# Optimization experiments

Measured on AMD Instinct MI355X. Metric: run time of the kernel, lower is better.

Reference implementation:

```python
import jax, jax.numpy as jnp
import numpy as np
import math

B, N, FIN, FOUT, OPE = 16, 2048, 128, 128, 64


def setup_inputs() -> dict:
    key = jax.random.key(0)
    ks = jax.random.split(key, 10)
    h = jax.random.normal(ks[0], (B, N, FIN), dtype=jnp.float32)
    adj = jax.random.randint(ks[1], (B, N, N), 0, 2).astype(jnp.float32)
    op_emb = jax.random.normal(ks[2], (B, N, OPE), dtype=jnp.float32)
    # Linear weights stored as (in, out) so y = x @ W; torch init scale ~ 1/sqrt(fan_in)
    s_in = 1.0 / math.sqrt(FIN)
    Wk = jax.random.uniform(ks[3], (FIN, FOUT), minval=-s_in, maxval=s_in)
    Wq = jax.random.uniform(ks[4], (FIN, FOUT), minval=-s_in, maxval=s_in)
    Wv = jax.random.uniform(ks[5], (FIN, FOUT), minval=-s_in, maxval=s_in)
    s_a = 1.0 / math.sqrt(FOUT)
    a_w = jax.random.uniform(ks[6], (FOUT,), minval=-s_a, maxval=s_a)
    s_op = 1.0 / math.sqrt(OPE)
    op_W = jax.random.uniform(ks[7], (OPE, FOUT), minval=-s_op, maxval=s_op)
    op_b = jax.random.uniform(ks[8], (FOUT,), minval=-s_op, maxval=s_op)
    ln_g = jnp.ones((FOUT,), dtype=jnp.float32)
    ln_b = jnp.zeros((FOUT,), dtype=jnp.float32)
    return {"h": h, "adj": adj, "op_emb": op_emb, "Wk": Wk, "Wq": Wq,
            "Wv": Wv, "a_w": a_w, "op_W": op_W, "op_b": op_b,
            "ln_g": ln_g, "ln_b": ln_b}


def reference(h, adj, op_emb, Wk, Wq, Wv, a_w, op_W, op_b, ln_g, ln_b):
    d = Wk.shape[1]
    Whk = h @ Wk  # (B,N,d)
    Whq = h @ Wq
    Whv = h @ Wv
    # Original builds a_input[b,e,l,m] = Whq[b,e,m]*Whk[b,l,m] (B,N,N,d) then
    # projects with a (d->1). Algebraically: scores[b,e,l] = <Whq[b,e], Whk[b,l]*a_w>.
    scores = jnp.einsum('bed,bld->bel', Whq, Whk * a_w)
    scores = scores / jnp.sqrt(jnp.float32(d))  # attention_rescale
    alpha = jax.nn.leaky_relu(scores, negative_slope=0.2)  # leakrelu
    alpha = alpha * adj  # multiplicative mask (zeros stay in the softmax)
    attn = jax.nn.softmax(alpha, axis=-1)  # softmax over source nodes l
    agg = jnp.einsum('bel,bld->bed', attn, Whv)  # (B,N,d)
    gate = jax.nn.sigmoid(op_emb @ op_W + op_b)  # opattention branch
    hp = gate * agg
    # LayerNorm over last dim, eps=1e-5
    mu = jnp.mean(hp, axis=-1, keepdims=True)
    var = jnp.mean(jnp.square(hp - mu), axis=-1, keepdims=True)
    return (hp - mu) * jax.lax.rsqrt(var + 1e-5) * ln_g + ln_b
```

## Files before the change

kernel.cpp:

```cpp
#include <hip/hip_runtime.h>

typedef unsigned int u32;
typedef float f32x4 __attribute__((ext_vector_type(4)));
typedef short s16x8 __attribute__((ext_vector_type(8)));

#define LDA 136

#define WQT_OFF 0ULL
#define WKT_OFF 32768ULL
#define WVT_OFF 65536ULL
#define OPWT_OFF 98304ULL
#define Q_OFF 114688ULL
#define K_OFF (Q_OFF + 8388608ULL)
#define VT_OFF (K_OFF + 8388608ULL)
#define GATE_OFF (VT_OFF + 8388608ULL)

__device__ __forceinline__ u32 f2bf(float f) {
  u32 u = __float_as_uint(f);
  return (u + 0x7fffu + ((u >> 16) & 1u)) >> 16;
}

__device__ __forceinline__ void gl_lds16(const void* g, void* l) {
  __builtin_amdgcn_global_load_lds((const __attribute__((address_space(1))) void*)g,
                                   (__attribute__((address_space(3))) void*)l, 16, 0, 0);
}

__global__ void k0_wt(const float* Wq, const float* Wk, const float* Wv,
                      const float* aw, const float* opW, char* ws) {
  int nt = blockIdx.x;
  int KK = (nt == 3) ? 64 : 128;
  const float* S = (nt == 0) ? Wq : (nt == 1) ? Wk : (nt == 2) ? Wv : opW;
  unsigned short* D = (unsigned short*)(ws + (nt == 0 ? WQT_OFF : nt == 1 ? WKT_OFF : nt == 2 ? WVT_OFF : OPWT_OFF));
  for (int i = threadIdx.x; i < 128 * KK; i += blockDim.x) {
    int d = i / KK, k = i - d * KK;
    float v = S[k * 128 + d];
    if (nt == 1) v *= aw[d] * 0.12751743f;
    D[i] = (unsigned short)f2bf(v);
  }
}

__launch_bounds__(256, 2)
__global__ void k1_proj(const float* __restrict__ h, const float* __restrict__ op_emb,
                        const float* __restrict__ op_b, char* __restrict__ ws) {
  int nt = blockIdx.x, et = blockIdx.y;
  int KK = (nt == 3) ? 64 : 128;
  __shared__ unsigned short bufA[128 * LDA];
  __shared__ unsigned short bufB[128 * LDA];
  unsigned short* wbuf = (nt == 2) ? bufB : bufA;
  unsigned short* xbuf = (nt == 2) ? bufA : bufB;
  const unsigned short* Wt = (const unsigned short*)(ws + (nt == 0 ? WQT_OFF : nt == 1 ? WKT_OFF : nt == 2 ? WVT_OFF : OPWT_OFF));
  {
    const u32* Ws = (const u32*)Wt;
    int cnt = 128 * KK / 2;
    for (int i = threadIdx.x; i < cnt; i += 256) {
      int r = (2 * i) / KK, c = 2 * i - r * KK;
      *(u32*)&wbuf[r * LDA + c] = Ws[i];
    }
  }
  {
    const float* X = (nt == 3) ? (op_emb + (size_t)et * 128 * 64) : (h + (size_t)et * 128 * 128);
    int cnt = 128 * KK / 4;
    for (int i = threadIdx.x; i < cnt; i += 256) {
      float4 v = *(const float4*)(X + 4 * i);
      int r = (4 * i) / KK, c = 4 * i - r * KK;
      u32 lo = f2bf(v.x) | (f2bf(v.y) << 16);
      u32 hi = f2bf(v.z) | (f2bf(v.w) << 16);
      *(uint2*)&xbuf[r * LDA + c] = make_uint2(lo, hi);
    }
  }
  __syncthreads();
  int tid = threadIdx.x, w = tid >> 6, lane = tid & 63, l15 = lane & 15, q = lane >> 4;
  int wa = w >> 1, wb = w & 1;
  f32x4 acc[4][4];
#pragma unroll
  for (int a = 0; a < 4; a++)
#pragma unroll
    for (int bq = 0; bq < 4; bq++) acc[a][bq] = f32x4{0.f, 0.f, 0.f, 0.f};
  for (int ks = 0; ks < KK / 32; ks++) {
    s16x8 af[4], bf_[4];
#pragma unroll
    for (int mt = 0; mt < 4; mt++)
      af[mt] = *(const s16x8*)&bufA[(wa * 64 + mt * 16 + l15) * LDA + ks * 32 + q * 8];
#pragma unroll
    for (int n2 = 0; n2 < 4; n2++)
      bf_[n2] = *(const s16x8*)&bufB[(wb * 64 + n2 * 16 + l15) * LDA + ks * 32 + q * 8];
#pragma unroll
    for (int mt = 0; mt < 4; mt++)
#pragma unroll
      for (int n2 = 0; n2 < 4; n2++)
        acc[mt][n2] = __builtin_amdgcn_mfma_f32_16x16x32_bf16(af[mt], bf_[n2], acc[mt][n2], 0, 0, 0);
  }
  if (nt <= 1) {
    unsigned short* Dst = (unsigned short*)(ws + (nt == 0 ? Q_OFF : K_OFF));
#pragma unroll
    for (int mt = 0; mt < 4; mt++)
#pragma unroll
      for (int n2 = 0; n2 < 4; n2++) {
        int d0 = wa * 64 + mt * 16 + q * 4;
        int eg = et * 128 + wb * 64 + n2 * 16 + l15;
        f32x4 a = acc[mt][n2];
        u32 lo = f2bf(a[0]) | (f2bf(a[1]) << 16);
        u32 hi = f2bf(a[2]) | (f2bf(a[3]) << 16);
        *(uint2*)(Dst + (size_t)eg * 128 + d0) = make_uint2(lo, hi);
      }
  } else if (nt == 2) {
    unsigned short* Dst = (unsigned short*)(ws + VT_OFF);
    int b = et >> 4;
    int ein0 = (et & 15) * 128;
#pragma unroll
    for (int mt = 0; mt < 4; mt++)
#pragma unroll
      for (int n2 = 0; n2 < 4; n2++) {
        int e0b = ein0 + wa * 64 + mt * 16 + q * 4;
        int d = wb * 64 + n2 * 16 + l15;
        f32x4 a = acc[mt][n2];
        u32 lo = f2bf(a[0]) | (f2bf(a[1]) << 16);
        u32 hi = f2bf(a[2]) | (f2bf(a[3]) << 16);
        *(uint2*)(Dst + (size_t)b * 128 * 2048 + (size_t)d * 2048 + e0b) = make_uint2(lo, hi);
      }
  } else {
    float* Dst = (float*)(ws + GATE_OFF);
#pragma unroll
    for (int mt = 0; mt < 4; mt++)
#pragma unroll
      for (int n2 = 0; n2 < 4; n2++) {
        int d0 = wa * 64 + mt * 16 + q * 4;
        int eg = et * 128 + wb * 64 + n2 * 16 + l15;
        f32x4 a = acc[mt][n2];
        float4 g4;
        g4.x = 1.f / (1.f + __builtin_amdgcn_exp2f(-(a[0] + op_b[d0 + 0]) * 1.4426950f));
        g4.y = 1.f / (1.f + __builtin_amdgcn_exp2f(-(a[1] + op_b[d0 + 1]) * 1.4426950f));
        g4.z = 1.f / (1.f + __builtin_amdgcn_exp2f(-(a[2] + op_b[d0 + 2]) * 1.4426950f));
        g4.w = 1.f / (1.f + __builtin_amdgcn_exp2f(-(a[3] + op_b[d0 + 3]) * 1.4426950f));
        *(float4*)(Dst + (size_t)eg * 128 + d0) = g4;
      }
  }
}

__launch_bounds__(512, 2)
__global__ void k2_attn(const float* __restrict__ adj, const float* __restrict__ ln_g,
                        const float* __restrict__ ln_b, char* __restrict__ ws,
                        float* __restrict__ out) {
  __shared__ char smem[100864];
  unsigned short* Klds = (unsigned short*)smem;
  unsigned short* Vlds = (unsigned short*)(smem + 32768);
  char* PLb = smem + 65536;
  float* sden = (float*)(smem + 100352);

  const int bid = blockIdx.x;
  const int xcd = bid & 7, slot = bid >> 3;
  const int b = xcd * 2 + (slot >> 4);
  const int e0 = (slot & 15) << 7;

  const unsigned short* Qg = (const unsigned short*)(ws + Q_OFF) + ((size_t)b * 2048 + e0) * 128;
  const unsigned short* Kg = (const unsigned short*)(ws + K_OFF) + (size_t)b * 2048 * 128;
  const unsigned short* Vtg = (const unsigned short*)(ws + VT_OFF) + (size_t)b * 128 * 2048;
  const float* gateg = (const float*)(ws + GATE_OFF) + ((size_t)b * 2048 + e0) * 128;
  const float* adjg = adj + (size_t)b * 2048 * 2048 + (size_t)e0 * 2048;

  const int tid = threadIdx.x;
  const int w = tid >> 6, lane = tid & 63, l15 = lane & 15, q = lane >> 4;
  const int wh = w >> 2, we = w & 3;

  if (tid < 128) sden[tid] = 0.0f;

  s16x8 qf[2][4];
#pragma unroll
  for (int et = 0; et < 2; et++) {
    const int e = we * 32 + et * 16 + l15;
#pragma unroll
    for (int ks = 0; ks < 4; ks++)
      qf[et][ks] = *(const s16x8*)(Qg + (size_t)e * 128 + ks * 32 + q * 8);
  }

  f32x4 oacc[4][2];
#pragma unroll
  for (int dt = 0; dt < 4; dt++)
#pragma unroll
    for (int et = 0; et < 2; et++) oacc[dt][et] = f32x4{0.f, 0.f, 0.f, 0.f};
  float dp0 = 0.0f, dp1 = 0.0f;
  float4 adjA[2][4], adjB[2][4];

#pragma unroll
  for (int j = 0; j < 4; j++) {
    int S = (j * 8 + w) * 64 + lane;
    int r = S >> 4, cp = S & 15, c = cp ^ (r & 15);
    gl_lds16(Kg + (size_t)r * 128 + (c << 3), (char*)Klds + (j * 8 + w) * 1024);
    gl_lds16(Vtg + (size_t)r * 2048 + (c << 3), (char*)Vlds + (j * 8 + w) * 1024);
  }
#pragma unroll
  for (int et = 0; et < 2; et++) {
    const int e = we * 32 + et * 16 + l15;
#pragma unroll
    for (int lt = 0; lt < 4; lt++)
      adjA[et][lt] = *(const float4*)(adjg + (size_t)e * 2048 + wh * 64 + lt * 16 + q * 4);
  }

#pragma unroll 2
  for (int it = 0; it < 16; it++) {
    __syncthreads();
    if (it < 15) {
      const float* ab = adjg + (it + 1) * 128;
#pragma unroll
      for (int et = 0; et < 2; et++) {
        const int e = we * 32 + et * 16 + l15;
#pragma unroll
        for (int lt = 0; lt < 4; lt++)
          adjB[et][lt] = *(const float4*)(ab + (size_t)e * 2048 + wh * 64 + lt * 16 + q * 4);
      }
    }
    f32x4 sacc[4][2];
#pragma unroll
    for (int lt = 0; lt < 4; lt++)
#pragma unroll
      for (int et = 0; et < 2; et++) sacc[lt][et] = f32x4{0.f, 0.f, 0.f, 0.f};
#pragma unroll
    for (int ks = 0; ks < 4; ks++) {
      s16x8 kf[4];
#pragma unroll
      for (int lt = 0; lt < 4; lt++) {
        int l = wh * 64 + lt * 16 + l15;
        kf[lt] = *(const s16x8*)((char*)Klds + l * 256 + (((ks * 4 + q) ^ l15) << 4));
      }
#pragma unroll
      for (int lt = 0; lt < 4; lt++)
#pragma unroll
        for (int et = 0; et < 2; et++)
          sacc[lt][et] = __builtin_amdgcn_mfma_f32_16x16x32_bf16(kf[lt], qf[et][ks], sacc[lt][et], 0, 0, 0);
    }
#pragma unroll
    for (int et = 0; et < 2; et++) {
      const int e = we * 32 + et * 16 + l15;
#pragma unroll
      for (int lt = 0; lt < 4; lt++) {
        float4 aj = adjA[et][lt];
        f32x4 s = sacc[lt][et];
        float p0 = __builtin_amdgcn_exp2f(fmaxf(s[0], 0.2f * s[0]) * aj.x);
        float p1 = __builtin_amdgcn_exp2f(fmaxf(s[1], 0.2f * s[1]) * aj.y);
        float p2 = __builtin_amdgcn_exp2f(fmaxf(s[2], 0.2f * s[2]) * aj.z);
        float p3 = __builtin_amdgcn_exp2f(fmaxf(s[3], 0.2f * s[3]) * aj.w);
        float sum4 = (p0 + p1) + (p2 + p3);
        if (et == 0) dp0 += sum4; else dp1 += sum4;
        u32 lo = f2bf(p0) | (f2bf(p1) << 16);
        u32 hi = f2bf(p2) | (f2bf(p3) << 16);
        *(uint2*)(PLb + (size_t)e * 272 + ((wh * 64 + lt * 16 + q * 4) << 1)) = make_uint2(lo, hi);
      }
    }
    __syncthreads();
    if (it < 15) {
      const unsigned short* kb = Kg + (size_t)(it + 1) * 128 * 128;
#pragma unroll
      for (int j = 0; j < 4; j++) {
        int S = (j * 8 + w) * 64 + lane;
        int r = S >> 4, cp = S & 15, c = cp ^ (r & 15);
        gl_lds16(kb + (size_t)r * 128 + (c << 3), (char*)Klds + (j * 8 + w) * 1024);
      }
    }
#pragma unroll
    for (int ks = 0; ks < 4; ks++) {
      s16x8 vf[4], pf[2];
#pragma unroll
      for (int dt = 0; dt < 4; dt++) {
        int d = wh * 64 + dt * 16 + l15;
        vf[dt] = *(const s16x8*)((char*)Vlds + d * 256 + (((ks * 4 + q) ^ l15) << 4));
      }
#pragma unroll
      for (int et = 0; et < 2; et++) {
        const int e = we * 32 + et * 16 + l15;
        pf[et] = *(const s16x8*)(PLb + (size_t)e * 272 + ks * 64 + q * 16);
      }
#pragma unroll
      for (int dt = 0; dt < 4; dt++)
#pragma unroll
        for (int et = 0; et < 2; et++)
          oacc[dt][et] = __builtin_amdgcn_mfma_f32_16x16x32_bf16(vf[dt], pf[et], oacc[dt][et], 0, 0, 0);
    }
    __syncthreads();
    if (it < 15) {
      const unsigned short* vb = Vtg + (size_t)(it + 1) * 128;
#pragma unroll
      for (int j = 0; j < 4; j++) {
        int S = (j * 8 + w) * 64 + lane;
        int r = S >> 4, cp = S & 15, c = cp ^ (r & 15);
        gl_lds16(vb + (size_t)r * 2048 + (c << 3), (char*)Vlds + (j * 8 + w) * 1024);
      }
#pragma unroll
      for (int et = 0; et < 2; et++)
#pragma unroll
        for (int lt = 0; lt < 4; lt++) adjA[et][lt] = adjB[et][lt];
    }
  }

  atomicAdd(&sden[we * 32 + l15], dp0);
  atomicAdd(&sden[we * 32 + 16 + l15], dp1);
  __syncthreads();
  const float inv0 = 1.0f / sden[we * 32 + l15];
  const float inv1 = 1.0f / sden[we * 32 + 16 + l15];
  float* O2 = (float*)smem;
#pragma unroll
  for (int dt = 0; dt < 4; dt++)
#pragma unroll
    for (int et = 0; et < 2; et++) {
      const int e = we * 32 + et * 16 + l15;
      const int d0 = wh * 64 + dt * 16 + q * 4;
      f32x4 v = oacc[dt][et];
      const float inv = et ? inv1 : inv0;
      float4 o;
      o.x = v[0] * inv; o.y = v[1] * inv; o.z = v[2] * inv; o.w = v[3] * inv;
      *(float4*)(O2 + e * 132 + d0) = o;
    }
  __syncthreads();
  {
    const int e = tid >> 2, j = tid & 3;
    const float* row = O2 + e * 132 + j * 32;
    const float* gr = gateg + (size_t)e * 128 + j * 32;
    float4 x[8];
    float s1 = 0.f, s2 = 0.f;
#pragma unroll
    for (int i = 0; i < 8; i++) {
      float4 v = *(const float4*)(row + i * 4);
      float4 g = *(const float4*)(gr + i * 4);
      float4 hp;
      hp.x = v.x * g.x; hp.y = v.y * g.y; hp.z = v.z * g.z; hp.w = v.w * g.w;
      x[i] = hp;
      s1 += (hp.x + hp.y) + (hp.z + hp.w);
      s2 += (hp.x * hp.x + hp.y * hp.y) + (hp.z * hp.z + hp.w * hp.w);
    }
    s1 += __shfl_xor(s1, 1); s2 += __shfl_xor(s2, 1);
    s1 += __shfl_xor(s1, 2); s2 += __shfl_xor(s2, 2);
    const float mu = s1 * 0.0078125f;
    const float var = s2 * 0.0078125f - mu * mu;
    const float rs = rsqrtf(var + 1e-5f);
    float* orow = out + ((size_t)b * 2048 + e0 + e) * 128 + j * 32;
    const float* gg = ln_g + j * 32;
    const float* bb = ln_b + j * 32;
#pragma unroll
    for (int i = 0; i < 8; i++) {
      float4 gv = *(const float4*)(gg + i * 4);
      float4 bv = *(const float4*)(bb + i * 4);
      float4 o;
      o.x = (x[i].x - mu) * rs * gv.x + bv.x;
      o.y = (x[i].y - mu) * rs * gv.y + bv.y;
      o.z = (x[i].z - mu) * rs * gv.z + bv.z;
      o.w = (x[i].w - mu) * rs * gv.w + bv.w;
      *(float4*)(orow + i * 4) = o;
    }
  }
}

extern "C" void kernel_launch(void* const* d_in, const int* in_sizes, int n_in,
                              void* d_out, int out_size, void* d_ws, size_t ws_size,
                              hipStream_t stream) {
  const float* h = (const float*)d_in[0];
  const float* adj = (const float*)d_in[1];
  const float* op_emb = (const float*)d_in[2];
  const float* Wk = (const float*)d_in[3];
  const float* Wq = (const float*)d_in[4];
  const float* Wv = (const float*)d_in[5];
  const float* a_w = (const float*)d_in[6];
  const float* op_W = (const float*)d_in[7];
  const float* op_b = (const float*)d_in[8];
  const float* ln_g = (const float*)d_in[9];
  const float* ln_b = (const float*)d_in[10];
  char* ws = (char*)d_ws;
  float* out = (float*)d_out;

  k0_wt<<<4, 256, 0, stream>>>(Wq, Wk, Wv, a_w, op_W, ws);
  k1_proj<<<dim3(4, 256), 256, 0, stream>>>(h, op_emb, op_b, ws);
  k2_attn<<<256, 512, 0, stream>>>(adj, ln_g, ln_b, ws, out);
}
```

Measured before the change: 490.5 us.

## Double-buffer K/V tiles and keep P in per-wave LDS for PV MFMA

The attention kernel now double-buffers K and V tiles in LDS so the next tile's loads overlap the current compute, which drops two of the three barriers per iteration. Each wave stages its probability tile in a private LDS region, so the P·V product needs no block-wide sync. The PV accumulation is split along the source dimension across the two wave halves and reduced through LDS at the end. The weight-transpose kernel is spread over more blocks and the projection kernel uses shifts and wider 16-byte weight copies. The cost is about 150KB of LDS per block, which likely cuts occupancy to one block per CU, and twice as many output accumulator registers.

```diff
diff --git a/kernel.cpp b/kernel.cpp
--- a/kernel.cpp
+++ b/kernel.cpp
@@ -27,15 +27,17 @@
 
 __global__ void k0_wt(const float* Wq, const float* Wk, const float* Wv,
                       const float* aw, const float* opW, char* ws) {
-  int nt = blockIdx.x;
-  int KK = (nt == 3) ? 64 : 128;
+  int nt = blockIdx.x, part = blockIdx.y;
+  int kksh = (nt == 3) ? 6 : 7;
+  int KK = 1 << kksh;
   const float* S = (nt == 0) ? Wq : (nt == 1) ? Wk : (nt == 2) ? Wv : opW;
   unsigned short* D = (unsigned short*)(ws + (nt == 0 ? WQT_OFF : nt == 1 ? WKT_OFF : nt == 2 ? WVT_OFF : OPWT_OFF));
-  for (int i = threadIdx.x; i < 128 * KK; i += blockDim.x) {
-    int d = i / KK, k = i - d * KK;
+  int base = part * 8 * KK;
+  for (int i = threadIdx.x; i < 8 * KK; i += 256) {
+    int d = part * 8 + (i >> kksh), k = i & (KK - 1);
     float v = S[k * 128 + d];
     if (nt == 1) v *= aw[d] * 0.12751743f;
-    D[i] = (unsigned short)f2bf(v);
+    D[base + i] = (unsigned short)f2bf(v);
   }
 }
 
@@ -43,18 +45,20 @@
 __global__ void k1_proj(const float* __restrict__ h, const float* __restrict__ op_emb,
                         const float* __restrict__ op_b, char* __restrict__ ws) {
   int nt = blockIdx.x, et = blockIdx.y;
-  int KK = (nt == 3) ? 64 : 128;
+  int kksh = (nt == 3) ? 6 : 7;
+  int KK = 1 << kksh;
   __shared__ unsigned short bufA[128 * LDA];
   __shared__ unsigned short bufB[128 * LDA];
   unsigned short* wbuf = (nt == 2) ? bufB : bufA;
   unsigned short* xbuf = (nt == 2) ? bufA : bufB;
   const unsigned short* Wt = (const unsigned short*)(ws + (nt == 0 ? WQT_OFF : nt == 1 ? WKT_OFF : nt == 2 ? WVT_OFF : OPWT_OFF));
   {
-    const u32* Ws = (const u32*)Wt;
-    int cnt = 128 * KK / 2;
+    const uint4* Ws = (const uint4*)Wt;
+    int cnt = 128 * KK / 8;
     for (int i = threadIdx.x; i < cnt; i += 256) {
-      int r = (2 * i) / KK, c = 2 * i - r * KK;
-      *(u32*)&wbuf[r * LDA + c] = Ws[i];
+      uint4 v = Ws[i];
+      int r = (8 * i) >> kksh, c = (8 * i) & (KK - 1);
+      *(uint4*)&wbuf[r * LDA + c] = v;
     }
   }
   {
@@ -62,7 +66,7 @@
     int cnt = 128 * KK / 4;
     for (int i = threadIdx.x; i < cnt; i += 256) {
       float4 v = *(const float4*)(X + 4 * i);
-      int r = (4 * i) / KK, c = 4 * i - r * KK;
+      int r = (4 * i) >> kksh, c = (4 * i) & (KK - 1);
       u32 lo = f2bf(v.x) | (f2bf(v.y) << 16);
       u32 hi = f2bf(v.z) | (f2bf(v.w) << 16);
       *(uint2*)&xbuf[r * LDA + c] = make_uint2(lo, hi);
@@ -141,11 +145,8 @@
 __global__ void k2_attn(const float* __restrict__ adj, const float* __restrict__ ln_g,
                         const float* __restrict__ ln_b, char* __restrict__ ws,
                         float* __restrict__ out) {
-  __shared__ char smem[100864];
-  unsigned short* Klds = (unsigned short*)smem;
-  unsigned short* Vlds = (unsigned short*)(smem + 32768);
-  char* PLb = smem + 65536;
-  float* sden = (float*)(smem + 100352);
+  __shared__ char smem[150016];
+  float* sden = (float*)(smem + 149504);
 
   const int bid = blockIdx.x;
   const int xcd = bid & 7, slot = bid >> 3;
@@ -161,6 +162,7 @@
   const int tid = threadIdx.x;
   const int w = tid >> 6, lane = tid & 63, l15 = lane & 15, q = lane >> 4;
   const int wh = w >> 2, we = w & 3;
+  char* PLw = smem + 131072 + w * 2304;
 
   if (tid < 128) sden[tid] = 0.0f;
 
@@ -173,34 +175,54 @@
       qf[et][ks] = *(const s16x8*)(Qg + (size_t)e * 128 + ks * 32 + q * 8);
   }
 
-  f32x4 oacc[4][2];
-#pragma unroll
-  for (int dt = 0; dt < 4; dt++)
-#pragma unroll
-    for (int et = 0; et < 2; et++) oacc[dt][et] = f32x4{0.f, 0.f, 0.f, 0.f};
+  f32x4 oacc[2][8];
+#pragma unroll
+  for (int et = 0; et < 2; et++)
+#pragma unroll
+    for (int nt = 0; nt < 8; nt++) oacc[et][nt] = f32x4{0.f, 0.f, 0.f, 0.f};
   float dp0 = 0.0f, dp1 = 0.0f;
-  float4 adjA[2][4], adjB[2][4];
+  float4 adjB[2][4];
 
 #pragma unroll
   for (int j = 0; j < 4; j++) {
     int S = (j * 8 + w) * 64 + lane;
     int r = S >> 4, cp = S & 15, c = cp ^ (r & 15);
-    gl_lds16(Kg + (size_t)r * 128 + (c << 3), (char*)Klds + (j * 8 + w) * 1024);
-    gl_lds16(Vtg + (size_t)r * 2048 + (c << 3), (char*)Vlds + (j * 8 + w) * 1024);
+    gl_lds16(Kg + (size_t)r * 128 + (c << 3), smem + (j * 8 + w) * 1024);
+    gl_lds16(Vtg + (size_t)r * 2048 + (c << 3), smem + 65536 + (j * 8 + w) * 1024);
   }
 #pragma unroll
   for (int et = 0; et < 2; et++) {
     const int e = we * 32 + et * 16 + l15;
 #pragma unroll
     for (int lt = 0; lt < 4; lt++)
-      adjA[et][lt] = *(const float4*)(adjg + (size_t)e * 2048 + wh * 64 + lt * 16 + q * 4);
+      adjB[et][lt] = *(const float4*)(adjg + (size_t)e * 2048 + wh * 64 + lt * 16 + q * 4);
   }
 
 #pragma unroll 2
   for (int it = 0; it < 16; it++) {
     __syncthreads();
+    const int cur = it & 1, nxt = cur ^ 1;
+    char* Kl = smem + cur * 32768;
+    char* Vl = smem + 65536 + cur * 32768;
+    float4 adjA[2][4];
+#pragma unroll
+    for (int et = 0; et < 2; et++)
+#pragma unroll
+      for (int lt = 0; lt < 4; lt++) adjA[et][lt] = adjB[et][lt];
+
     if (it < 15) {
-      const float* ab = adjg + (it + 1) * 128;
+      const unsigned short* kb = Kg + (size_t)(it + 1) * 16384;
+      const unsigned short* vb = Vtg + (size_t)(it + 1) * 128;
+      char* Kd = smem + nxt * 32768;
+      char* Vd = smem + 65536 + nxt * 32768;
+#pragma unroll
+      for (int j = 0; j < 4; j++) {
+        int S = (j * 8 + w) * 64 + lane;
+        int r = S >> 4, cp = S & 15, c = cp ^ (r & 15);
+        gl_lds16(kb + (size_t)r * 128 + (c << 3), Kd + (j * 8 + w) * 1024);
+        gl_lds16(vb + (size_t)r * 2048 + (c << 3), Vd + (j * 8 + w) * 1024);
+      }
+      const float* ab = adjg + (size_t)(it + 1) * 128;
 #pragma unroll
       for (int et = 0; et < 2; et++) {
         const int e = we * 32 + et * 16 + l15;
@@ -209,6 +231,7 @@
           adjB[et][lt] = *(const float4*)(ab + (size_t)e * 2048 + wh * 64 + lt * 16 + q * 4);
       }
     }
+
     f32x4 sacc[4][2];
 #pragma unroll
     for (int lt = 0; lt < 4; lt++)
@@ -220,7 +243,7 @@
 #pragma unroll
       for (int lt = 0; lt < 4; lt++) {
         int l = wh * 64 + lt * 16 + l15;
-        kf[lt] = *(const s16x8*)((char*)Klds + l * 256 + (((ks * 4 + q) ^ l15) << 4));
+        kf[lt] = *(const s16x8*)(Kl + l * 256 + (((ks * 4 + q) ^ l15) << 4));
       }
 #pragma unroll
       for (int lt = 0; lt < 4; lt++)
@@ -228,9 +251,12 @@
         for (int et = 0; et < 2; et++)
           sacc[lt][et] = __builtin_amdgcn_mfma_f32_16x16x32_bf16(kf[lt], qf[et][ks], sacc[lt][et], 0, 0, 0);
     }
+
+    s16x8 af[2][2];
 #pragma unroll
     for (int et = 0; et < 2; et++) {
-      const int e = we * 32 + et * 16 + l15;
+      u32 pqw[4][2];
+      float dsum = 0.0f;
 #pragma unroll
       for (int lt = 0; lt < 4; lt++) {
         float4 aj = adjA[et][lt];
@@ -239,77 +265,71 @@
         float p1 = __builtin_amdgcn_exp2f(fmaxf(s[1], 0.2f * s[1]) * aj.y);
         float p2 = __builtin_amdgcn_exp2f(fmaxf(s[2], 0.2f * s[2]) * aj.z);
         float p3 = __builtin_amdgcn_exp2f(fmaxf(s[3], 0.2f * s[3]) * aj.w);
-        float sum4 = (p0 + p1) + (p2 + p3);
-        if (et == 0) dp0 += sum4; else dp1 += sum4;
-        u32 lo = f2bf(p0) | (f2bf(p1) << 16);
-        u32 hi = f2bf(p2) | (f2bf(p3) << 16);
-        *(uint2*)(PLb + (size_t)e * 272 + ((wh * 64 + lt * 16 + q * 4) << 1)) = make_uint2(lo, hi);
-      }
-    }
-    __syncthreads();
-    if (it < 15) {
-      const unsigned short* kb = Kg + (size_t)(it + 1) * 128 * 128;
-#pragma unroll
-      for (int j = 0; j < 4; j++) {
-        int S = (j * 8 + w) * 64 + lane;
-        int r = S >> 4, cp = S & 15, c = cp ^ (r & 15);
-        gl_lds16(kb + (size_t)r * 128 + (c << 3), (char*)Klds + (j * 8 + w) * 1024);
-      }
-    }
-#pragma unroll
-    for (int ks = 0; ks < 4; ks++) {
-      s16x8 vf[4], pf[2];
-#pragma unroll
-      for (int dt = 0; dt < 4; dt++) {
-        int d = wh * 64 + dt * 16 + l15;
-        vf[dt] = *(const s16x8*)((char*)Vlds + d * 256 + (((ks * 4 + q) ^ l15) << 4));
-      }
-#pragma unroll
-      for (int et = 0; et < 2; et++) {
-        const int e = we * 32 + et * 16 + l15;
-        pf[et] = *(const s16x8*)(PLb + (size_t)e * 272 + ks * 64 + q * 16);
-      }
-#pragma unroll
-      for (int dt = 0; dt < 4; dt++)
-#pragma unroll
-        for (int et = 0; et < 2; et++)
-          oacc[dt][et] = __builtin_amdgcn_mfma_f32_16x16x32_bf16(vf[dt], pf[et], oacc[dt][et], 0, 0, 0);
-    }
-    __syncthreads();
-    if (it < 15) {
-      const unsigned short* vb = Vtg + (size_t)(it + 1) * 128;
-#pragma unroll
-      for (int j = 0; j < 4; j++) {
-        int S = (j * 8 + w) * 64 + lane;
-        int r = S >> 4, cp = S & 15, c = cp ^ (r & 15);
-        gl_lds16(vb + (size_t)r * 2048 + (c << 3), (char*)Vlds + (j * 8 + w) * 1024);
+        dsum += (p0 + p1) + (p2 + p3);
+        pqw[lt][0] = f2bf(p0) | (f2bf(p1) << 16);
+        pqw[lt][1] = f2bf(p2) | (f2bf(p3) << 16);
+      }
+      if (et == 0) dp0 += dsum; else dp1 += dsum;
+#pragma unroll
+      for (int lt = 0; lt < 4; lt++)
+        *(uint2*)(PLw + l15 * 144 + lt * 32 + q * 8) = make_uint2(pqw[lt][0], pqw[lt][1]);
+      af[et][0] = *(const s16x8*)(PLw + l15 * 144 + q * 16);
+      af[et][1] = *(const s16x8*)(PLw + l15 * 144 + 64 + q * 16);
+    }
+
+#pragma unroll
+    for (int ks2 = 0; ks2 < 2; ks2++) {
+      s16x8 vf[8];
+#pragma unroll
+      for (int nt = 0; nt < 8; nt++) {
+        int d = nt * 16 + l15;
+        vf[nt] = *(const s16x8*)(Vl + d * 256 + (((wh * 8 + ks2 * 4 + q) ^ l15) << 4));
       }
 #pragma unroll
       for (int et = 0; et < 2; et++)
 #pragma unroll
-        for (int lt = 0; lt < 4; lt++) adjA[et][lt] = adjB[et][lt];
+        for (int nt = 0; nt < 8; nt++)
+          oacc[et][nt] = __builtin_amdgcn_mfma_f32_16x16x32_bf16(af[et][ks2], vf[nt], oacc[et][nt], 0, 0, 0);
     }
   }
 
   atomicAdd(&sden[we * 32 + l15], dp0);
   atomicAdd(&sden[we * 32 + 16 + l15], dp1);
   __syncthreads();
-  const float inv0 = 1.0f / sden[we * 32 + l15];
-  const float inv1 = 1.0f / sden[we * 32 + 16 + l15];
+
   float* O2 = (float*)smem;
-#pragma unroll
-  for (int dt = 0; dt < 4; dt++)
+  if (wh == 1) {
+#pragma unroll
+    for (int et = 0; et < 2; et++)
+#pragma unroll
+      for (int nt = 0; nt < 8; nt++) {
+        const int eb = we * 32 + et * 16 + q * 4;
+        const int d = nt * 16 + l15;
+#pragma unroll
+        for (int r = 0; r < 4; r++) O2[(eb + r) * 132 + d] = oacc[et][nt][r];
+      }
+  }
+  __syncthreads();
+  if (wh == 0) {
 #pragma unroll
     for (int et = 0; et < 2; et++) {
-      const int e = we * 32 + et * 16 + l15;
-      const int d0 = wh * 64 + dt * 16 + q * 4;
-      f32x4 v = oacc[dt][et];
-      const float inv = et ? inv1 : inv0;
-      float4 o;
-      o.x = v[0] * inv; o.y = v[1] * inv; o.z = v[2] * inv; o.w = v[3] * inv;
-      *(float4*)(O2 + e * 132 + d0) = o;
-    }
+      const int eb = we * 32 + et * 16 + q * 4;
+      float inv[4];
+#pragma unroll
+      for (int r = 0; r < 4; r++) inv[r] = 1.0f / sden[eb + r];
+#pragma unroll
+      for (int nt = 0; nt < 8; nt++) {
+        const int d = nt * 16 + l15;
+#pragma unroll
+        for (int r = 0; r < 4; r++) {
+          int idx = (eb + r) * 132 + d;
+          O2[idx] = (O2[idx] + oacc[et][nt][r]) * inv[r];
+        }
+      }
+    }
+  }
   __syncthreads();
+
   {
     const int e = tid >> 2, j = tid & 3;
     const float* row = O2 + e * 132 + j * 32;
@@ -365,7 +385,7 @@
   char* ws = (char*)d_ws;
   float* out = (float*)d_out;
 
-  k0_wt<<<4, 256, 0, stream>>>(Wq, Wk, Wv, a_w, op_W, ws);
+  k0_wt<<<dim3(4, 16), 256, 0, stream>>>(Wq, Wk, Wv, a_w, op_W, ws);
   k1_proj<<<dim3(4, 256), 256, 0, stream>>>(h, op_emb, op_b, ws);
   k2_attn<<<256, 512, 0, stream>>>(adj, ln_g, ln_b, ws, out);
 }
```

Result: faster. 468.3 us (-4.5%).
